# Kernel optimization log

Hardware: AMD Instinct MI355X
Metric: run time of the kernel (lower is better)

## Reference

```python
import jax, jax.numpy as jnp
import numpy as np

B, C, H, W = 8, 8, 512, 512


def setup_inputs() -> dict:
    key = jax.random.key(0)
    k1, k2 = jax.random.split(key)
    logits = jax.random.normal(k1, (B, C, H, W), dtype=jnp.float32)
    target = jax.random.normal(k2, (B, C, H, W), dtype=jnp.float32)
    return {"logits": logits, "target": target}


def _hausdorff_one(x, y):
    # x, y: [H, W] -> H points in R^W (rows are points), euclidean metric,
    # matching hausdorff.hausdorff_distance on a 2D array.
    x2 = jnp.sum(x * x, axis=-1)  # [H]
    y2 = jnp.sum(y * y, axis=-1)  # [H]
    # squared pairwise distances via GEMM identity; clamp negatives from fp error
    d2 = jnp.maximum(x2[:, None] + y2[None, :] - 2.0 * (x @ y.T), 0.0)  # [H, H]
    d = jnp.sqrt(d2)
    fwd = jnp.max(jnp.min(d, axis=1))  # sup_x inf_y
    bwd = jnp.max(jnp.min(d, axis=0))  # sup_y inf_x
    return jnp.maximum(fwd, bwd)


def reference(logits, target):
    lx = jnp.argmax(logits, axis=1).astype(jnp.float32)  # [B, H, W] label maps
    ty = jnp.argmax(target, axis=1).astype(jnp.float32)  # [B, H, W]
    hd = jax.vmap(_hausdorff_one)(lx, ty)  # [B]
    return jnp.mean(hd)
```

## Files before the change

kernel.cpp:

```cpp
#include <hip/hip_runtime.h>
#include <hip/hip_bf16.h>
#include <climits>

#define HWSZ 262144
#define CHWSZ 2097152

typedef short short8 __attribute__((ext_vector_type(8)));
typedef float f32x4 __attribute__((ext_vector_type(4)));
typedef float f4 __attribute__((ext_vector_type(4)));
typedef unsigned short u16x8 __attribute__((ext_vector_type(8)));

__global__ __launch_bounds__(256) void hd_argmax(const float* __restrict__ logits,
                                                 const float* __restrict__ target,
                                                 ushort* __restrict__ lxb,
                                                 ushort* __restrict__ tyb,
                                                 float* __restrict__ x2,
                                                 float* __restrict__ y2,
                                                 int* __restrict__ rowmin,
                                                 int* __restrict__ colmin) {
    int gid = blockIdx.x * 256 + threadIdx.x;
    if (gid < 4096) {
        rowmin[gid] = INT_MAX;
        colmin[gid] = INT_MAX;
    }
    int t = gid;
    int p = t << 3;
    int b = p >> 18;
    int off = p & (HWSZ - 1);
    int l = threadIdx.x & 63;
    int row = p >> 9;

    const f4* L = (const f4*)(logits + (size_t)b * CHWSZ + off);
    const f4* T = (const f4*)(target + (size_t)b * CHWSZ + off);

    {
        f4 v[16];
#pragma unroll
        for (int c = 0; c < 8; ++c) {
            v[2 * c]     = L[c * (HWSZ / 4)];
            v[2 * c + 1] = L[c * (HWSZ / 4) + 1];
        }
        u16x8 ub;
        int s = 0;
#pragma unroll
        for (int half = 0; half < 2; ++half) {
#pragma unroll
            for (int j = 0; j < 4; ++j) {
                float bv = v[half][j];
                int bi = 0;
#pragma unroll
                for (int c = 1; c < 8; ++c) {
                    float x = v[2 * c + half][j];
                    bool g = x > bv;
                    bv = g ? x : bv;
                    bi = g ? c : bi;
                }
                ub[half * 4 + j] = (ushort)(__float_as_uint((float)bi) >> 16);
                s += bi * bi;
            }
        }
        *(u16x8*)(lxb + p) = ub;
#pragma unroll
        for (int o = 32; o > 0; o >>= 1) s += __shfl_xor(s, o, 64);
        if (l == 0) x2[row] = (float)s;
    }
    {
        f4 w[16];
#pragma unroll
        for (int c = 0; c < 8; ++c) {
            w[2 * c]     = T[c * (HWSZ / 4)];
            w[2 * c + 1] = T[c * (HWSZ / 4) + 1];
        }
        u16x8 wb;
        int s = 0;
#pragma unroll
        for (int half = 0; half < 2; ++half) {
#pragma unroll
            for (int j = 0; j < 4; ++j) {
                float bv = w[half][j];
                int bi = 0;
#pragma unroll
                for (int c = 1; c < 8; ++c) {
                    float x = w[2 * c + half][j];
                    bool g = x > bv;
                    bv = g ? x : bv;
                    bi = g ? c : bi;
                }
                wb[half * 4 + j] = (ushort)(__float_as_uint((float)bi) >> 16);
                s += bi * bi;
            }
        }
        *(u16x8*)(tyb + p) = wb;
#pragma unroll
        for (int o = 32; o > 0; o >>= 1) s += __shfl_xor(s, o, 64);
        if (l == 0) y2[row] = (float)s;
    }
}

__global__ __launch_bounds__(256) void hd_dist(const ushort* __restrict__ lxb,
                                               const ushort* __restrict__ tyb,
                                               const float* __restrict__ x2,
                                               const float* __restrict__ y2,
                                               int* __restrict__ rowmin,
                                               int* __restrict__ colmin) {
    int b = blockIdx.y;
    int ti = blockIdx.x >> 3, tj = blockIdx.x & 7;
    int tid = threadIdx.x;
    int l = tid & 63;
    int wv = tid >> 6;
    int wr = wv >> 1, wc = wv & 1;
    int lr = l & 15, lg = l >> 4;

    const ushort* X = lxb + b * HWSZ + (ti * 64 + wr * 32 + lr) * 512 + lg * 8;
    const ushort* Y = tyb + b * HWSZ + (tj * 64 + wc * 32 + lr) * 512 + lg * 8;

    f32x4 acc00 = {0.f, 0.f, 0.f, 0.f};
    f32x4 acc01 = {0.f, 0.f, 0.f, 0.f};
    f32x4 acc10 = {0.f, 0.f, 0.f, 0.f};
    f32x4 acc11 = {0.f, 0.f, 0.f, 0.f};

#pragma unroll 4
    for (int kk = 0; kk < 512; kk += 32) {
        short8 a0 = *(const short8*)(X + kk);
        short8 a1 = *(const short8*)(X + 8192 + kk);
        short8 b0 = *(const short8*)(Y + kk);
        short8 b1 = *(const short8*)(Y + 8192 + kk);
        acc00 = __builtin_amdgcn_mfma_f32_16x16x32_bf16(a0, b0, acc00, 0, 0, 0);
        acc01 = __builtin_amdgcn_mfma_f32_16x16x32_bf16(a0, b1, acc01, 0, 0, 0);
        acc10 = __builtin_amdgcn_mfma_f32_16x16x32_bf16(a1, b0, acc10, 0, 0, 0);
        acc11 = __builtin_amdgcn_mfma_f32_16x16x32_bf16(a1, b1, acc11, 0, 0, 0);
    }

    int rb = (b << 9) + ti * 64 + wr * 32;
    int cb = (b << 9) + tj * 64 + wc * 32;
    float x2v0[4], x2v1[4];
#pragma unroll
    for (int r = 0; r < 4; ++r) {
        x2v0[r] = x2[rb + lg * 4 + r];
        x2v1[r] = x2[rb + 16 + lg * 4 + r];
    }
    float y2v0 = y2[cb + lr];
    float y2v1 = y2[cb + 16 + lr];

    int d2[2][2][4];
#pragma unroll
    for (int r = 0; r < 4; ++r) {
        d2[0][0][r] = (int)(fmaxf(fmaf(-2.0f, acc00[r], x2v0[r] + y2v0), 0.0f) + 0.5f);
        d2[0][1][r] = (int)(fmaxf(fmaf(-2.0f, acc01[r], x2v0[r] + y2v1), 0.0f) + 0.5f);
        d2[1][0][r] = (int)(fmaxf(fmaf(-2.0f, acc10[r], x2v1[r] + y2v0), 0.0f) + 0.5f);
        d2[1][1][r] = (int)(fmaxf(fmaf(-2.0f, acc11[r], x2v1[r] + y2v1), 0.0f) + 0.5f);
    }

#pragma unroll
    for (int fi = 0; fi < 2; ++fi) {
#pragma unroll
        for (int r = 0; r < 4; ++r) {
            int m = min(d2[fi][0][r], d2[fi][1][r]);
            m = min(m, __shfl_xor(m, 1, 64));
            m = min(m, __shfl_xor(m, 2, 64));
            m = min(m, __shfl_xor(m, 4, 64));
            m = min(m, __shfl_xor(m, 8, 64));
            if (lr == 0) atomicMin(&rowmin[rb + fi * 16 + lg * 4 + r], m);
        }
    }
#pragma unroll
    for (int fj = 0; fj < 2; ++fj) {
        int m;
        if (fj == 0) {
            m = min(min(min(d2[0][0][0], d2[0][0][1]), min(d2[0][0][2], d2[0][0][3])),
                    min(min(d2[1][0][0], d2[1][0][1]), min(d2[1][0][2], d2[1][0][3])));
        } else {
            m = min(min(min(d2[0][1][0], d2[0][1][1]), min(d2[0][1][2], d2[0][1][3])),
                    min(min(d2[1][1][0], d2[1][1][1]), min(d2[1][1][2], d2[1][1][3])));
        }
        m = min(m, __shfl_xor(m, 16, 64));
        m = min(m, __shfl_xor(m, 32, 64));
        if (lg == 0) atomicMin(&colmin[cb + fj * 16 + lr], m);
    }
}

__global__ __launch_bounds__(512) void hd_final(const int* __restrict__ rowmin,
                                                const int* __restrict__ colmin,
                                                float* __restrict__ out) {
    int w = threadIdx.x >> 6, l = threadIdx.x & 63;
    int m = 0;
#pragma unroll
    for (int j = 0; j < 512; j += 64) {
        m = max(m, rowmin[(w << 9) + j + l]);
        m = max(m, colmin[(w << 9) + j + l]);
    }
#pragma unroll
    for (int s = 32; s > 0; s >>= 1) m = max(m, __shfl_xor(m, s, 64));
    __shared__ float hd[8];
    if (l == 0) hd[w] = sqrtf((float)m);
    __syncthreads();
    if (threadIdx.x == 0) {
        float s = 0.0f;
#pragma unroll
        for (int i = 0; i < 8; ++i) s += hd[i];
        out[0] = s * 0.125f;
    }
}

extern "C" void kernel_launch(void* const* d_in, const int* in_sizes, int n_in,
                              void* d_out, int out_size, void* d_ws, size_t ws_size,
                              hipStream_t stream) {
    (void)in_sizes; (void)n_in; (void)out_size; (void)ws_size;
    const float* logits = (const float*)d_in[0];
    const float* target = (const float*)d_in[1];

    char* ws = (char*)d_ws;
    ushort* lxb = (ushort*)ws;
    ushort* tyb = (ushort*)(ws + (4u << 20));
    float* x2   = (float*)(ws + (8u << 20));
    float* y2   = x2 + 4096;
    int* rowmin = (int*)(y2 + 4096);
    int* colmin = rowmin + 4096;
    float* out  = (float*)d_out;

    hipLaunchKernelGGL(hd_argmax, dim3(1024),  dim3(256), 0, stream,
                       logits, target, lxb, tyb, x2, y2, rowmin, colmin);
    hipLaunchKernelGGL(hd_dist,   dim3(64, 8), dim3(256), 0, stream,
                       lxb, tyb, x2, y2, rowmin, colmin);
    hipLaunchKernelGGL(hd_final,  dim3(1),     dim3(512), 0, stream, rowmin, colmin, out);
}
```

Baseline: 51.07 us.

## Use int8 label maps with i8 MFMA and fold final reduction into dist kernel

Label maps are stored as int8 bytes instead of bf16, and the distance GEMM uses the integer 16x16x64 i8 MFMA with exact integer squared distances. This halves the intermediate memory traffic and halves the number of MFMA issues. The separate final-reduction kernel is removed: a global atomic counter lets the last hd_dist block do the max/sqrt/mean, saving one launch at the cost of a threadfence and an atomic per block.

New measurement: 70.69 us. 1.38x slower.

```diff
diff --git a/kernel.cpp b/kernel.cpp
--- a/kernel.cpp
+++ b/kernel.cpp
@@ -1,28 +1,27 @@
 #include <hip/hip_runtime.h>
-#include <hip/hip_bf16.h>
 #include <climits>
 
 #define HWSZ 262144
 #define CHWSZ 2097152
 
-typedef short short8 __attribute__((ext_vector_type(8)));
-typedef float f32x4 __attribute__((ext_vector_type(4)));
+typedef int i32x4 __attribute__((ext_vector_type(4)));
 typedef float f4 __attribute__((ext_vector_type(4)));
-typedef unsigned short u16x8 __attribute__((ext_vector_type(8)));
 
 __global__ __launch_bounds__(256) void hd_argmax(const float* __restrict__ logits,
                                                  const float* __restrict__ target,
-                                                 ushort* __restrict__ lxb,
-                                                 ushort* __restrict__ tyb,
-                                                 float* __restrict__ x2,
-                                                 float* __restrict__ y2,
+                                                 unsigned char* __restrict__ lxb,
+                                                 unsigned char* __restrict__ tyb,
+                                                 int* __restrict__ x2,
+                                                 int* __restrict__ y2,
                                                  int* __restrict__ rowmin,
-                                                 int* __restrict__ colmin) {
+                                                 int* __restrict__ colmin,
+                                                 int* __restrict__ counter) {
     int gid = blockIdx.x * 256 + threadIdx.x;
     if (gid < 4096) {
         rowmin[gid] = INT_MAX;
         colmin[gid] = INT_MAX;
     }
+    if (gid == 4096) counter[0] = 0;
     int t = gid;
     int p = t << 3;
     int b = p >> 18;
@@ -40,7 +39,7 @@
             v[2 * c]     = L[c * (HWSZ / 4)];
             v[2 * c + 1] = L[c * (HWSZ / 4) + 1];
         }
-        u16x8 ub;
+        unsigned long long pk = 0;
         int s = 0;
 #pragma unroll
         for (int half = 0; half < 2; ++half) {
@@ -55,14 +54,14 @@
                     bv = g ? x : bv;
                     bi = g ? c : bi;
                 }
-                ub[half * 4 + j] = (ushort)(__float_as_uint((float)bi) >> 16);
+                pk |= (unsigned long long)bi << (8 * (half * 4 + j));
                 s += bi * bi;
             }
         }
-        *(u16x8*)(lxb + p) = ub;
+        *(unsigned long long*)(lxb + p) = pk;
 #pragma unroll
         for (int o = 32; o > 0; o >>= 1) s += __shfl_xor(s, o, 64);
-        if (l == 0) x2[row] = (float)s;
+        if (l == 0) x2[row] = s;
     }
     {
         f4 w[16];
@@ -71,7 +70,7 @@
             w[2 * c]     = T[c * (HWSZ / 4)];
             w[2 * c + 1] = T[c * (HWSZ / 4) + 1];
         }
-        u16x8 wb;
+        unsigned long long pk = 0;
         int s = 0;
 #pragma unroll
         for (int half = 0; half < 2; ++half) {
@@ -86,23 +85,25 @@
                     bv = g ? x : bv;
                     bi = g ? c : bi;
                 }
-                wb[half * 4 + j] = (ushort)(__float_as_uint((float)bi) >> 16);
+                pk |= (unsigned long long)bi << (8 * (half * 4 + j));
                 s += bi * bi;
             }
         }
-        *(u16x8*)(tyb + p) = wb;
+        *(unsigned long long*)(tyb + p) = pk;
 #pragma unroll
         for (int o = 32; o > 0; o >>= 1) s += __shfl_xor(s, o, 64);
-        if (l == 0) y2[row] = (float)s;
+        if (l == 0) y2[row] = s;
     }
 }
 
-__global__ __launch_bounds__(256) void hd_dist(const ushort* __restrict__ lxb,
-                                               const ushort* __restrict__ tyb,
-                                               const float* __restrict__ x2,
-                                               const float* __restrict__ y2,
+__global__ __launch_bounds__(256) void hd_dist(const unsigned char* __restrict__ lxb,
+                                               const unsigned char* __restrict__ tyb,
+                                               const int* __restrict__ x2,
+                                               const int* __restrict__ y2,
                                                int* __restrict__ rowmin,
-                                               int* __restrict__ colmin) {
+                                               int* __restrict__ colmin,
+                                               int* __restrict__ counter,
+                                               float* __restrict__ out) {
     int b = blockIdx.y;
     int ti = blockIdx.x >> 3, tj = blockIdx.x & 7;
     int tid = threadIdx.x;
@@ -111,44 +112,44 @@
     int wr = wv >> 1, wc = wv & 1;
     int lr = l & 15, lg = l >> 4;
 
-    const ushort* X = lxb + b * HWSZ + (ti * 64 + wr * 32 + lr) * 512 + lg * 8;
-    const ushort* Y = tyb + b * HWSZ + (tj * 64 + wc * 32 + lr) * 512 + lg * 8;
-
-    f32x4 acc00 = {0.f, 0.f, 0.f, 0.f};
-    f32x4 acc01 = {0.f, 0.f, 0.f, 0.f};
-    f32x4 acc10 = {0.f, 0.f, 0.f, 0.f};
-    f32x4 acc11 = {0.f, 0.f, 0.f, 0.f};
-
-#pragma unroll 4
-    for (int kk = 0; kk < 512; kk += 32) {
-        short8 a0 = *(const short8*)(X + kk);
-        short8 a1 = *(const short8*)(X + 8192 + kk);
-        short8 b0 = *(const short8*)(Y + kk);
-        short8 b1 = *(const short8*)(Y + 8192 + kk);
-        acc00 = __builtin_amdgcn_mfma_f32_16x16x32_bf16(a0, b0, acc00, 0, 0, 0);
-        acc01 = __builtin_amdgcn_mfma_f32_16x16x32_bf16(a0, b1, acc01, 0, 0, 0);
-        acc10 = __builtin_amdgcn_mfma_f32_16x16x32_bf16(a1, b0, acc10, 0, 0, 0);
-        acc11 = __builtin_amdgcn_mfma_f32_16x16x32_bf16(a1, b1, acc11, 0, 0, 0);
+    const unsigned char* X = lxb + b * HWSZ + (ti * 64 + wr * 32 + lr) * 512 + lg * 16;
+    const unsigned char* Y = tyb + b * HWSZ + (tj * 64 + wc * 32 + lr) * 512 + lg * 16;
+
+    i32x4 acc00 = {0, 0, 0, 0};
+    i32x4 acc01 = {0, 0, 0, 0};
+    i32x4 acc10 = {0, 0, 0, 0};
+    i32x4 acc11 = {0, 0, 0, 0};
+
+#pragma unroll
+    for (int kk = 0; kk < 512; kk += 64) {
+        i32x4 a0 = *(const i32x4*)(X + kk);
+        i32x4 a1 = *(const i32x4*)(X + 8192 + kk);
+        i32x4 b0 = *(const i32x4*)(Y + kk);
+        i32x4 b1 = *(const i32x4*)(Y + 8192 + kk);
+        acc00 = __builtin_amdgcn_mfma_i32_16x16x64_i8(a0, b0, acc00, 0, 0, 0);
+        acc01 = __builtin_amdgcn_mfma_i32_16x16x64_i8(a0, b1, acc01, 0, 0, 0);
+        acc10 = __builtin_amdgcn_mfma_i32_16x16x64_i8(a1, b0, acc10, 0, 0, 0);
+        acc11 = __builtin_amdgcn_mfma_i32_16x16x64_i8(a1, b1, acc11, 0, 0, 0);
     }
 
     int rb = (b << 9) + ti * 64 + wr * 32;
     int cb = (b << 9) + tj * 64 + wc * 32;
-    float x2v0[4], x2v1[4];
+    int x2v0[4], x2v1[4];
 #pragma unroll
     for (int r = 0; r < 4; ++r) {
         x2v0[r] = x2[rb + lg * 4 + r];
         x2v1[r] = x2[rb + 16 + lg * 4 + r];
     }
-    float y2v0 = y2[cb + lr];
-    float y2v1 = y2[cb + 16 + lr];
+    int y2v0 = y2[cb + lr];
+    int y2v1 = y2[cb + 16 + lr];
 
     int d2[2][2][4];
 #pragma unroll
     for (int r = 0; r < 4; ++r) {
-        d2[0][0][r] = (int)(fmaxf(fmaf(-2.0f, acc00[r], x2v0[r] + y2v0), 0.0f) + 0.5f);
-        d2[0][1][r] = (int)(fmaxf(fmaf(-2.0f, acc01[r], x2v0[r] + y2v1), 0.0f) + 0.5f);
-        d2[1][0][r] = (int)(fmaxf(fmaf(-2.0f, acc10[r], x2v1[r] + y2v0), 0.0f) + 0.5f);
-        d2[1][1][r] = (int)(fmaxf(fmaf(-2.0f, acc11[r], x2v1[r] + y2v1), 0.0f) + 0.5f);
+        d2[0][0][r] = x2v0[r] + y2v0 - 2 * acc00[r];
+        d2[0][1][r] = x2v0[r] + y2v1 - 2 * acc01[r];
+        d2[1][0][r] = x2v1[r] + y2v0 - 2 * acc10[r];
+        d2[1][1][r] = x2v1[r] + y2v1 - 2 * acc11[r];
     }
 
 #pragma unroll
@@ -177,28 +178,35 @@
         m = min(m, __shfl_xor(m, 32, 64));
         if (lg == 0) atomicMin(&colmin[cb + fj * 16 + lr], m);
     }
-}
-
-__global__ __launch_bounds__(512) void hd_final(const int* __restrict__ rowmin,
-                                                const int* __restrict__ colmin,
-                                                float* __restrict__ out) {
-    int w = threadIdx.x >> 6, l = threadIdx.x & 63;
-    int m = 0;
-#pragma unroll
-    for (int j = 0; j < 512; j += 64) {
-        m = max(m, rowmin[(w << 9) + j + l]);
-        m = max(m, colmin[(w << 9) + j + l]);
-    }
-#pragma unroll
-    for (int s = 32; s > 0; s >>= 1) m = max(m, __shfl_xor(m, s, 64));
-    __shared__ float hd[8];
-    if (l == 0) hd[w] = sqrtf((float)m);
+
+    __threadfence();
+    __shared__ int islast;
+    if (tid == 0) islast = (atomicAdd(counter, 1) == 511);
     __syncthreads();
-    if (threadIdx.x == 0) {
-        float s = 0.0f;
-#pragma unroll
-        for (int i = 0; i < 8; ++i) s += hd[i];
-        out[0] = s * 0.125f;
+    if (islast) {
+        __threadfence();
+        int bt = tid >> 5;
+        int q = tid & 31;
+        int m = 0;
+#pragma unroll
+        for (int j = 0; j < 512; j += 32) {
+            m = max(m, rowmin[(bt << 9) + j + q]);
+            m = max(m, colmin[(bt << 9) + j + q]);
+        }
+        m = max(m, __shfl_xor(m, 1, 64));
+        m = max(m, __shfl_xor(m, 2, 64));
+        m = max(m, __shfl_xor(m, 4, 64));
+        m = max(m, __shfl_xor(m, 8, 64));
+        m = max(m, __shfl_xor(m, 16, 64));
+        __shared__ float hd[8];
+        if (q == 0) hd[bt] = sqrtf((float)m);
+        __syncthreads();
+        if (tid == 0) {
+            float s = 0.0f;
+#pragma unroll
+            for (int i = 0; i < 8; ++i) s += hd[i];
+            out[0] = s * 0.125f;
+        }
     }
 }
 
@@ -210,17 +218,17 @@
     const float* target = (const float*)d_in[1];
 
     char* ws = (char*)d_ws;
-    ushort* lxb = (ushort*)ws;
-    ushort* tyb = (ushort*)(ws + (4u << 20));
-    float* x2   = (float*)(ws + (8u << 20));
-    float* y2   = x2 + 4096;
-    int* rowmin = (int*)(y2 + 4096);
+    unsigned char* lxb = (unsigned char*)ws;
+    unsigned char* tyb = (unsigned char*)(ws + (2u << 20));
+    int* x2     = (int*)(ws + (4u << 20));
+    int* y2     = x2 + 4096;
+    int* rowmin = y2 + 4096;
     int* colmin = rowmin + 4096;
+    int* counter = colmin + 4096;
     float* out  = (float*)d_out;
 
     hipLaunchKernelGGL(hd_argmax, dim3(1024),  dim3(256), 0, stream,
-                       logits, target, lxb, tyb, x2, y2, rowmin, colmin);
+                       logits, target, lxb, tyb, x2, y2, rowmin, colmin, counter);
     hipLaunchKernelGGL(hd_dist,   dim3(64, 8), dim3(256), 0, stream,
-                       lxb, tyb, x2, y2, rowmin, colmin);
-    hipLaunchKernelGGL(hd_final,  dim3(1),     dim3(512), 0, stream, rowmin, colmin, out);
+                       lxb, tyb, x2, y2, rowmin, colmin, counter, out);
 }
```
